# Optimization experiments

Hardware: AMD Instinct MI355X
Metric: run time of the kernel (lower is better)

Reference implementation:

```python
import jax, jax.numpy as jnp
import numpy as np

THETA = 1.0
V_TH = 1.0       # spikingjelly IFNode default v_threshold
SG_ALPHA = 4.0   # spikingjelly surrogate.Sigmoid default alpha


@jax.custom_vjp
def heaviside(x):
    # spike = 1 if membrane - threshold >= 0
    return (x >= 0).astype(x.dtype)

def _heaviside_fwd(x):
    return (x >= 0).astype(x.dtype), x

def _heaviside_bwd(x, g):
    s = jax.nn.sigmoid(SG_ALPHA * x)
    return (g * SG_ALPHA * s * (1.0 - s),)

heaviside.defvjp(_heaviside_fwd, _heaviside_bwd)


@jax.custom_vjp
def spike_aggregate(spike_out, z_total):
    return spike_out

def _sa_fwd(spike_out, z_total):
    return spike_out, z_total

def _sa_bwd(z_total, g):
    surrogate = (z_total > 0).astype(g.dtype) / THETA
    return (jnp.zeros_like(g), g * surrogate)

spike_aggregate.defvjp(_sa_fwd, _sa_bwd)


def setup_inputs() -> dict:
    key = jax.random.key(0)
    k_x, k_w1, k_b1, k_w2, k_b2 = jax.random.split(key, 5)
    B, D_in, H, D_out = 4096, 784, 800, 10
    x = jax.random.uniform(k_x, (B, D_in), dtype=jnp.float32)
    # nn.Linear-style init: U(-1/sqrt(fan_in), 1/sqrt(fan_in))
    s1 = 1.0 / np.sqrt(D_in)
    s2 = 1.0 / np.sqrt(H)
    W1 = jax.random.uniform(k_w1, (H, D_in), jnp.float32, -s1, s1)
    b1 = jax.random.uniform(k_b1, (H,), jnp.float32, -s1, s1)
    W2 = jax.random.uniform(k_w2, (D_out, H), jnp.float32, -s2, s2)
    b2 = jax.random.uniform(k_b2, (D_out,), jnp.float32, -s2, s2)
    return {"x": x, "W1": W1, "b1": b1, "W2": W2, "b2": b2, "T_sim": 32}


def reference(x, W1, b1, W2, b2, T_sim):
    B = x.shape[0]
    x = x.reshape(B, -1)
    # fixed Bernoulli rate encoding (rand_like(x) < x)
    u = jax.random.uniform(jax.random.key(42), x.shape, dtype=x.dtype)
    x_fixed = (u < x).astype(x.dtype)
    # fc1 input is the same every timestep -> compute once
    cur1 = x_fixed @ W1.T + b1                     # [B, 800]

    def step(carry, _):
        v1, v2, count, z_total = carry
        h1 = v1 + cur1
        spk1 = heaviside(h1 - V_TH)
        v1 = h1 * (1.0 - jax.lax.stop_gradient(spk1))  # hard reset to 0, detach_reset
        cur2 = spk1 @ W2.T + b2                    # [B, 10]
        z_total = z_total + cur2
        h2 = v2 + cur2
        spk2 = heaviside(h2 - V_TH)
        v2 = h2 * (1.0 - jax.lax.stop_gradient(spk2))
        count = count + spk2
        return (v1, v2, count, z_total), None

    H, D_out = W1.shape[0], W2.shape[0]
    init = (jnp.zeros((B, H), x.dtype), jnp.zeros((B, D_out), x.dtype),
            jnp.zeros((B, D_out), x.dtype), jnp.zeros((B, D_out), x.dtype))
    (v1, v2, count, z_total), _ = jax.lax.scan(step, init, None, length=T_sim)
    return spike_aggregate(count, z_total)
```

## Files before the change

kernel.cpp:

```cpp
#include <hip/hip_runtime.h>
#include <stdint.h>

#define B_ROWS 4096
#define D_IN   784
#define H_DIM  800
#define D_OUT  10
#define T_SIM  32
#define N_ELEM (B_ROWS * D_IN)
#define CAP    512

__device__ __forceinline__ void threefry2x32(uint32_t k0, uint32_t k1,
                                             uint32_t& x0, uint32_t& x1) {
  uint32_t ks0 = k0, ks1 = k1, ks2 = k0 ^ k1 ^ 0x1BD11BDAu;
  x0 += ks0; x1 += ks1;
#define TF_RND(r) { x0 += x1; x1 = (x1 << (r)) | (x1 >> (32 - (r))); x1 ^= x0; }
  TF_RND(13) TF_RND(15) TF_RND(26) TF_RND(6)
  x0 += ks1; x1 += ks2 + 1u;
  TF_RND(17) TF_RND(29) TF_RND(16) TF_RND(24)
  x0 += ks2; x1 += ks0 + 2u;
  TF_RND(13) TF_RND(15) TF_RND(26) TF_RND(6)
  x0 += ks0; x1 += ks1 + 3u;
  TF_RND(17) TF_RND(29) TF_RND(16) TF_RND(24)
  x0 += ks1; x1 += ks2 + 4u;
  TF_RND(13) TF_RND(15) TF_RND(26) TF_RND(6)
  x0 += ks2; x1 += ks0 + 5u;
#undef TF_RND
}

__global__ __launch_bounds__(256) void gen_xfixed(const float* __restrict__ x,
                                                  float* __restrict__ xf) {
  int i = blockIdx.x * blockDim.x + threadIdx.x;
  if (i >= N_ELEM) return;
  uint32_t c0 = 0u, c1 = (uint32_t)i;
  threefry2x32(0u, 42u, c0, c1);
  uint32_t bits = c0 ^ c1;
  float u = __uint_as_float((bits >> 9) | 0x3F800000u) - 1.0f;
  xf[i] = (u < x[i]) ? 1.0f : 0.0f;
}

#define BM 128
#define BN 64
#define BK 16

__global__ __launch_bounds__(256) void gemm_periods(const float* __restrict__ xf,
                                                    const float* __restrict__ W1,
                                                    const float* __restrict__ b1,
                                                    uint8_t* __restrict__ pb) {
  __shared__ __align__(16) float As[BK][BM + 4];
  __shared__ __align__(16) float Bs[BK][BN + 4];
  const int m0 = blockIdx.y * BM;
  const int n0 = blockIdx.x * BN;
  const int t  = threadIdx.x;
  const int tx = t & 15, ty = t >> 4;
  const int ar = t >> 1;
  const int ak = (t & 1) * 8;
  const int br = t >> 2;
  const int bk = (t & 3) * 4;
  const int hB = n0 + br;
  const bool bOK = (hB < H_DIM);
  const float* aptr = xf + (m0 + ar) * D_IN + ak;
  const float* bptr = W1 + (bOK ? hB : 0) * D_IN + bk;

  float4 a0 = *(const float4*)(aptr);
  float4 a1 = *(const float4*)(aptr + 4);
  float4 b0 = *(const float4*)(bptr);
  if (!bOK) { b0.x = b0.y = b0.z = b0.w = 0.0f; }

  float acc[8][4] = {};
  for (int kt = 0; kt < D_IN; kt += BK) {
    As[ak + 0][ar] = a0.x; As[ak + 1][ar] = a0.y;
    As[ak + 2][ar] = a0.z; As[ak + 3][ar] = a0.w;
    As[ak + 4][ar] = a1.x; As[ak + 5][ar] = a1.y;
    As[ak + 6][ar] = a1.z; As[ak + 7][ar] = a1.w;
    Bs[bk + 0][br] = b0.x; Bs[bk + 1][br] = b0.y;
    Bs[bk + 2][br] = b0.z; Bs[bk + 3][br] = b0.w;
    __syncthreads();
    if (kt + BK < D_IN) {
      a0 = *(const float4*)(aptr + kt + BK);
      a1 = *(const float4*)(aptr + kt + BK + 4);
      b0 = *(const float4*)(bptr + kt + BK);
      if (!bOK) { b0.x = b0.y = b0.z = b0.w = 0.0f; }
    }
#pragma unroll
    for (int kk = 0; kk < BK; kk++) {
      float4 av0 = *(const float4*)&As[kk][ty * 8];
      float4 av1 = *(const float4*)&As[kk][ty * 8 + 4];
      float4 bv  = *(const float4*)&Bs[kk][tx * 4];
      float a[8] = {av0.x, av0.y, av0.z, av0.w, av1.x, av1.y, av1.z, av1.w};
      float b[4] = {bv.x, bv.y, bv.z, bv.w};
#pragma unroll
      for (int mi = 0; mi < 8; mi++)
#pragma unroll
        for (int ni = 0; ni < 4; ni++)
          acc[mi][ni] = __builtin_fmaf(a[mi], b[ni], acc[mi][ni]);
    }
    __syncthreads();
  }
  const int hOut = n0 + tx * 4;
  if (hOut < H_DIM) {
    float4 bb = *(const float4*)&b1[hOut];
#pragma unroll
    for (int mi = 0; mi < 8; mi++) {
      int m = m0 + ty * 8 + mi;
      float c4[4] = {acc[mi][0] + bb.x, acc[mi][1] + bb.y,
                     acc[mi][2] + bb.z, acc[mi][3] + bb.w};
      uint32_t packed = 0;
#pragma unroll
      for (int ni = 0; ni < 4; ni++) {
        float c = c4[ni];
        float v = 0.0f;
        int p = 0;
#pragma unroll 1
        for (int s = 1; s <= T_SIM; s++) {
          float h1 = v + c;
          if (h1 >= 1.0f) { p = s; break; }
          v = h1;
        }
        packed |= (uint32_t)p << (8 * ni);
      }
      *(uint32_t*)&pb[(size_t)m * H_DIM + hOut] = packed;
    }
  }
}

__global__ __launch_bounds__(640) void snn_scan(const uint8_t* __restrict__ pb,
                                                const float* __restrict__ W2,
                                                const float* __restrict__ b2,
                                                float* __restrict__ out) {
  __shared__ __align__(8) uint32_t mkS[2][CAP];
  __shared__ uint16_t hidxS[2][CAP];
  __shared__ __align__(16) float wst[2 * 5 * (CAP / 2) * 4];
  __shared__ int      lenS[2];
  __shared__ uint32_t mtbl[T_SIM + 1];
  __shared__ float    c2s[2][T_SIM][D_OUT];
  __shared__ float    b2f[D_OUT];
  const int tid  = threadIdx.x;
  const int row0 = blockIdx.x * 2;

  if (tid <= T_SIM) {
    uint32_t mk = 0;
    if (tid) for (int s = tid; s <= T_SIM; s += tid) mk |= 1u << (s - 1);
    mtbl[tid] = mk;
  }
  if (tid < D_OUT) b2f[tid] = b2[tid];
  __syncthreads();

  if (tid < 128) {
    const int r = tid >> 6, ln = tid & 63;
    const uint64_t lm = (1ull << ln) - 1ull;
    const uint8_t* prow = pb + (size_t)(row0 + r) * H_DIM;
    uint8_t pv[13];
#pragma unroll
    for (int ch = 0; ch < 13; ++ch) {
      int h = ch * 64 + ln;
      pv[ch] = (h < H_DIM) ? prow[h] : (uint8_t)0;
    }
    int off = 0;
#pragma unroll
    for (int ch = 0; ch < 13; ++ch) {
      bool g = (pv[ch] != 0);
      uint64_t bal = __ballot(g);
      int pos = off + __popcll(bal & lm);
      if (g && pos < CAP) {
        hidxS[r][pos] = (uint16_t)(ch * 64 + ln);
        mkS[r][pos]   = mtbl[pv[ch]];
      }
      off += __popcll(bal);
    }
    if (ln == 0) lenS[r] = off;
  }
  __syncthreads();

  const int L0 = min(lenS[0], CAP), L1 = min(lenS[1], CAP);
  const bool ovf = (lenS[0] > CAP) || (lenS[1] > CAP);
  const int Lpad = (max(L0, L1) + 63) & ~63;

  for (int e = tid; e < 2 * CAP; e += 640) {
    int r = e >= CAP ? 1 : 0, i = e - r * CAP;
    if (i >= (r ? L1 : L0)) mkS[r][i] = 0u;
  }
  __syncthreads();

  {
    const int npairs = Lpad >> 1;
    for (int e = tid; e < 10 * npairs * 2; e += 640) {
      int tmpe = e;
      int hi = tmpe & 1; tmpe >>= 1;
      int i2 = tmpe % npairs; tmpe /= npairs;
      int j = tmpe % 5;  int r = tmpe / 5;
      const int o = 2 * j + hi;
      const int Lr = r ? L1 : L0;
      float2 w;
      int i0 = 2 * i2;
      w.x = (i0     < Lr) ? W2[o * H_DIM + hidxS[r][i0]]     : 0.0f;
      w.y = (i0 + 1 < Lr) ? W2[o * H_DIM + hidxS[r][i0 + 1]] : 0.0f;
      *(float2*)&wst[((r * 5 + j) * (CAP / 2) + i2) * 4 + hi * 2] = w;
    }
  }
  __syncthreads();

  {
    const int wv = tid >> 6;
    const int r = wv & 1, j = wv >> 1;
    const int lane = tid & 63;
    const int t = lane & 31;
    const int hi = lane >> 5;
    float s = 0.0f;
    if (!ovf) {
      const uint32_t* mbase = mkS[r];
      const float* wbase = &wst[(r * 5 + j) * (CAP / 2) * 4 + hi * 2];
      const int npairs = Lpad >> 1;
#pragma unroll 4
      for (int i2 = 0; i2 < npairs; ++i2) {
        uint2 mk2 = *(const uint2*)&mbase[2 * i2];
        float2 w2 = *(const float2*)(wbase + i2 * 4);
        float g0 = (float)((mk2.x >> t) & 1u);
        s = __builtin_fmaf(g0, w2.x, s);
        float g1 = (float)((mk2.y >> t) & 1u);
        s = __builtin_fmaf(g1, w2.y, s);
      }
    } else {
      const uint8_t* prow = pb + (size_t)(row0 + r) * H_DIM;
      const int o = 2 * j + hi;
      const uint32_t vbit = 1u << t;
      for (int h = 0; h < H_DIM; ++h) {
        uint32_t mk = mtbl[prow[h]];
        float w = W2[o * H_DIM + h];
        s += (mk & vbit) ? w : 0.0f;
      }
    }
    c2s[r][t][2 * j + hi] = s;
  }
  __syncthreads();

  if (tid < 2 * D_OUT) {
    const int r = tid / D_OUT, o = tid % D_OUT;
    const float bb = b2f[o];
    float v = 0.0f; int cnt = 0;
#pragma unroll
    for (int t = 0; t < T_SIM; ++t) {
      float cur2 = c2s[r][t][o] + bb;
      float h2 = v + cur2;
      bool spk = (h2 >= 1.0f);
      cnt += spk ? 1 : 0;
      v = spk ? 0.0f : h2;
    }
    out[(size_t)(row0 + r) * D_OUT + o] = (float)cnt;
  }
}

extern "C" void kernel_launch(void* const* d_in, const int* in_sizes, int n_in,
                              void* d_out, int out_size, void* d_ws, size_t ws_size,
                              hipStream_t stream) {
  const float* x  = (const float*)d_in[0];
  const float* W1 = (const float*)d_in[1];
  const float* b1 = (const float*)d_in[2];
  const float* W2 = (const float*)d_in[3];
  const float* b2 = (const float*)d_in[4];
  float* outp = (float*)d_out;

  float*   xf = (float*)d_ws;
  uint8_t* pbuf = (uint8_t*)(xf + N_ELEM);

  gen_xfixed<<<N_ELEM / 256, 256, 0, stream>>>(x, xf);

  dim3 g1((H_DIM + BN - 1) / BN, B_ROWS / BM);
  gemm_periods<<<g1, 256, 0, stream>>>(xf, W1, b1, pbuf);

  snn_scan<<<B_ROWS / 2, 640, 0, stream>>>(pbuf, W2, b2, outp);
}
```

Before: 315.7 us.

## Shrink GEMM tile and restructure SNN scan with shared transposed W2

The GEMM tile drops from 128x64 to 64x64 with a 4x4 per-thread microtile, which doubles the number of blocks for better CU occupancy at the cost of less register reuse. The scan kernel now uses 320 threads. Each block stages a transposed copy of W2 in shared memory and stores packed (byte offset, spike mask) pairs, so each lane accumulates two outputs per active neuron. This replaces the earlier separate gather of W2 into a staging buffer. Each block now loads all of W2 (32 KB of LDS), which may limit occupancy.

```diff
diff --git a/kernel.cpp b/kernel.cpp
--- a/kernel.cpp
+++ b/kernel.cpp
@@ -38,7 +38,7 @@
   xf[i] = (u < x[i]) ? 1.0f : 0.0f;
 }
 
-#define BM 128
+#define BM 64
 #define BN 64
 #define BK 16
 
@@ -52,44 +52,37 @@
   const int n0 = blockIdx.x * BN;
   const int t  = threadIdx.x;
   const int tx = t & 15, ty = t >> 4;
-  const int ar = t >> 1;
-  const int ak = (t & 1) * 8;
-  const int br = t >> 2;
-  const int bk = (t & 3) * 4;
-  const int hB = n0 + br;
+  const int sM = t >> 2;
+  const int sK = (t & 3) * 4;
+  const int hB = n0 + sM;
   const bool bOK = (hB < H_DIM);
-  const float* aptr = xf + (m0 + ar) * D_IN + ak;
-  const float* bptr = W1 + (bOK ? hB : 0) * D_IN + bk;
-
-  float4 a0 = *(const float4*)(aptr);
-  float4 a1 = *(const float4*)(aptr + 4);
-  float4 b0 = *(const float4*)(bptr);
-  if (!bOK) { b0.x = b0.y = b0.z = b0.w = 0.0f; }
-
-  float acc[8][4] = {};
+  const float* aptr = xf + (m0 + sM) * D_IN + sK;
+  const float* bptr = W1 + (bOK ? hB : 0) * D_IN + sK;
+
+  float4 a4 = *(const float4*)(aptr);
+  float4 b4 = *(const float4*)(bptr);
+  if (!bOK) { b4.x = b4.y = b4.z = b4.w = 0.0f; }
+
+  float acc[4][4] = {};
   for (int kt = 0; kt < D_IN; kt += BK) {
-    As[ak + 0][ar] = a0.x; As[ak + 1][ar] = a0.y;
-    As[ak + 2][ar] = a0.z; As[ak + 3][ar] = a0.w;
-    As[ak + 4][ar] = a1.x; As[ak + 5][ar] = a1.y;
-    As[ak + 6][ar] = a1.z; As[ak + 7][ar] = a1.w;
-    Bs[bk + 0][br] = b0.x; Bs[bk + 1][br] = b0.y;
-    Bs[bk + 2][br] = b0.z; Bs[bk + 3][br] = b0.w;
+    As[sK + 0][sM] = a4.x; As[sK + 1][sM] = a4.y;
+    As[sK + 2][sM] = a4.z; As[sK + 3][sM] = a4.w;
+    Bs[sK + 0][sM] = b4.x; Bs[sK + 1][sM] = b4.y;
+    Bs[sK + 2][sM] = b4.z; Bs[sK + 3][sM] = b4.w;
     __syncthreads();
     if (kt + BK < D_IN) {
-      a0 = *(const float4*)(aptr + kt + BK);
-      a1 = *(const float4*)(aptr + kt + BK + 4);
-      b0 = *(const float4*)(bptr + kt + BK);
-      if (!bOK) { b0.x = b0.y = b0.z = b0.w = 0.0f; }
+      a4 = *(const float4*)(aptr + kt + BK);
+      b4 = *(const float4*)(bptr + kt + BK);
+      if (!bOK) { b4.x = b4.y = b4.z = b4.w = 0.0f; }
     }
 #pragma unroll
     for (int kk = 0; kk < BK; kk++) {
-      float4 av0 = *(const float4*)&As[kk][ty * 8];
-      float4 av1 = *(const float4*)&As[kk][ty * 8 + 4];
-      float4 bv  = *(const float4*)&Bs[kk][tx * 4];
-      float a[8] = {av0.x, av0.y, av0.z, av0.w, av1.x, av1.y, av1.z, av1.w};
+      float4 av = *(const float4*)&As[kk][ty * 4];
+      float4 bv = *(const float4*)&Bs[kk][tx * 4];
+      float a[4] = {av.x, av.y, av.z, av.w};
       float b[4] = {bv.x, bv.y, bv.z, bv.w};
 #pragma unroll
-      for (int mi = 0; mi < 8; mi++)
+      for (int mi = 0; mi < 4; mi++)
 #pragma unroll
         for (int ni = 0; ni < 4; ni++)
           acc[mi][ni] = __builtin_fmaf(a[mi], b[ni], acc[mi][ni]);
@@ -100,8 +93,8 @@
   if (hOut < H_DIM) {
     float4 bb = *(const float4*)&b1[hOut];
 #pragma unroll
-    for (int mi = 0; mi < 8; mi++) {
-      int m = m0 + ty * 8 + mi;
+    for (int mi = 0; mi < 4; mi++) {
+      int m = m0 + ty * 4 + mi;
       float c4[4] = {acc[mi][0] + bb.x, acc[mi][1] + bb.y,
                      acc[mi][2] + bb.z, acc[mi][3] + bb.w};
       uint32_t packed = 0;
@@ -123,13 +116,12 @@
   }
 }
 
-__global__ __launch_bounds__(640) void snn_scan(const uint8_t* __restrict__ pb,
+__global__ __launch_bounds__(320) void snn_scan(const uint8_t* __restrict__ pb,
                                                 const float* __restrict__ W2,
                                                 const float* __restrict__ b2,
                                                 float* __restrict__ out) {
-  __shared__ __align__(8) uint32_t mkS[2][CAP];
-  __shared__ uint16_t hidxS[2][CAP];
-  __shared__ __align__(16) float wst[2 * 5 * (CAP / 2) * 4];
+  __shared__ __align__(16) float W2T[H_DIM * D_OUT];
+  __shared__ __align__(8) uint2 pkS[2][CAP];
   __shared__ int      lenS[2];
   __shared__ uint32_t mtbl[T_SIM + 1];
   __shared__ float    c2s[2][T_SIM][D_OUT];
@@ -162,12 +154,19 @@
       uint64_t bal = __ballot(g);
       int pos = off + __popcll(bal & lm);
       if (g && pos < CAP) {
-        hidxS[r][pos] = (uint16_t)(ch * 64 + ln);
-        mkS[r][pos]   = mtbl[pv[ch]];
+        uint2 pk;
+        pk.x = (uint32_t)((ch * 64 + ln) * 40);
+        pk.y = mtbl[pv[ch]];
+        pkS[r][pos] = pk;
       }
       off += __popcll(bal);
     }
     if (ln == 0) lenS[r] = off;
+  } else {
+    for (int e = tid - 128; e < H_DIM * D_OUT; e += 192) {
+      int o = e / H_DIM, h = e - o * H_DIM;
+      W2T[h * D_OUT + o] = W2[e];
+    }
   }
   __syncthreads();
 
@@ -175,61 +174,41 @@
   const bool ovf = (lenS[0] > CAP) || (lenS[1] > CAP);
   const int Lpad = (max(L0, L1) + 63) & ~63;
 
-  for (int e = tid; e < 2 * CAP; e += 640) {
+  for (int e = tid; e < 2 * CAP; e += 320) {
     int r = e >= CAP ? 1 : 0, i = e - r * CAP;
-    if (i >= (r ? L1 : L0)) mkS[r][i] = 0u;
+    if (i >= (r ? L1 : L0) && i < Lpad) { pkS[r][i].x = 0u; pkS[r][i].y = 0u; }
   }
   __syncthreads();
 
   {
-    const int npairs = Lpad >> 1;
-    for (int e = tid; e < 10 * npairs * 2; e += 640) {
-      int tmpe = e;
-      int hi = tmpe & 1; tmpe >>= 1;
-      int i2 = tmpe % npairs; tmpe /= npairs;
-      int j = tmpe % 5;  int r = tmpe / 5;
-      const int o = 2 * j + hi;
-      const int Lr = r ? L1 : L0;
-      float2 w;
-      int i0 = 2 * i2;
-      w.x = (i0     < Lr) ? W2[o * H_DIM + hidxS[r][i0]]     : 0.0f;
-      w.y = (i0 + 1 < Lr) ? W2[o * H_DIM + hidxS[r][i0 + 1]] : 0.0f;
-      *(float2*)&wst[((r * 5 + j) * (CAP / 2) + i2) * 4 + hi * 2] = w;
-    }
-  }
-  __syncthreads();
-
-  {
-    const int wv = tid >> 6;
-    const int r = wv & 1, j = wv >> 1;
+    const int j = tid >> 6;
     const int lane = tid & 63;
     const int t = lane & 31;
-    const int hi = lane >> 5;
-    float s = 0.0f;
+    const int r = lane >> 5;
+    float s0 = 0.0f, s1 = 0.0f;
     if (!ovf) {
-      const uint32_t* mbase = mkS[r];
-      const float* wbase = &wst[(r * 5 + j) * (CAP / 2) * 4 + hi * 2];
-      const int npairs = Lpad >> 1;
+      const uint2* pp = pkS[r];
+      const char* wbase = (const char*)W2T + 8 * j;
 #pragma unroll 4
-      for (int i2 = 0; i2 < npairs; ++i2) {
-        uint2 mk2 = *(const uint2*)&mbase[2 * i2];
-        float2 w2 = *(const float2*)(wbase + i2 * 4);
-        float g0 = (float)((mk2.x >> t) & 1u);
-        s = __builtin_fmaf(g0, w2.x, s);
-        float g1 = (float)((mk2.y >> t) & 1u);
-        s = __builtin_fmaf(g1, w2.y, s);
+      for (int i = 0; i < Lpad; ++i) {
+        uint2 pk = pp[i];
+        float2 w = *(const float2*)(wbase + pk.x);
+        bool g = (pk.y >> t) & 1u;
+        s0 += g ? w.x : 0.0f;
+        s1 += g ? w.y : 0.0f;
       }
     } else {
       const uint8_t* prow = pb + (size_t)(row0 + r) * H_DIM;
-      const int o = 2 * j + hi;
       const uint32_t vbit = 1u << t;
       for (int h = 0; h < H_DIM; ++h) {
         uint32_t mk = mtbl[prow[h]];
-        float w = W2[o * H_DIM + h];
-        s += (mk & vbit) ? w : 0.0f;
-      }
-    }
-    c2s[r][t][2 * j + hi] = s;
+        float2 w = *(const float2*)&W2T[h * D_OUT + 2 * j];
+        s0 += (mk & vbit) ? w.x : 0.0f;
+        s1 += (mk & vbit) ? w.y : 0.0f;
+      }
+    }
+    c2s[r][t][2 * j]     = s0;
+    c2s[r][t][2 * j + 1] = s1;
   }
   __syncthreads();
 
@@ -267,5 +246,5 @@
   dim3 g1((H_DIM + BN - 1) / BN, B_ROWS / BM);
   gemm_periods<<<g1, 256, 0, stream>>>(xf, W1, b1, pbuf);
 
-  snn_scan<<<B_ROWS / 2, 640, 0, stream>>>(pbuf, W2, b2, outp);
-}
+  snn_scan<<<B_ROWS / 2, 320, 0, stream>>>(pbuf, W2, b2, outp);
+}
```

Result: faster. 286.4 us (-9.3%).
